# Kernel optimization log

Hardware: AMD Instinct MI355X
Metric: run time of the kernel (lower is better)

The kernel has to match this reference:

```python
import jax, jax.numpy as jnp
from jax import lax
import numpy as np

B, C, T = 16, 512, 4096
COEFF_INIT = 0.04


def setup_inputs() -> dict:
    key = jax.random.key(0)
    k1, k2 = jax.random.split(key)
    x = jax.random.normal(k1, (B, C, T), dtype=jnp.float32)
    # learned per-channel smoothing coefficients, initialized like the module
    weights = jnp.ones((C,), dtype=jnp.float32) * COEFF_INIT
    return {"x": x, "weights": weights}


def reference(x, weights):
    # clamp weights to [0, 1] (mirrors the in-place no-grad clamp; values stay
    # unchanged here since coeff_init is inside the range)
    s = jnp.clip(weights, 0.0, 1.0)  # [C]
    xt = jnp.moveaxis(x, 2, 0)       # [T, B, C]
    init = xt[0]                      # y_0 = x_0

    def step(acc, sample):
        acc = s * sample + (1.0 - s) * acc
        return acc, acc

    _, ys = lax.scan(step, init, xt[1:])          # [T-1, B, C]
    out = jnp.concatenate([init[None], ys], axis=0)  # [T, B, C]
    return jnp.moveaxis(out, 0, 2)                   # [B, C, T]
```

## Files before the change

kernel.cpp:

```cpp
#include <hip/hip_runtime.h>


constexpr int T_LEN = 4096;
constexpr int C_LEN = 512;
constexpr int BLOCK = 256;
constexpr int PER_THREAD = T_LEN / BLOCK;

__global__ __launch_bounds__(BLOCK) void ema_scan_kernel(
    const float* __restrict__ x,
    const float* __restrict__ w,
    float* __restrict__ y)
{
    const int row  = blockIdx.x;
    const int c    = row & (C_LEN - 1);
    const int tid  = threadIdx.x;
    const int lane = tid & 63;
    const int wave = tid >> 6;

    float s = w[c];
    s = fminf(fmaxf(s, 0.0f), 1.0f);
    const float a = 1.0f - s;

    const float* xr = x + (size_t)row * T_LEN + tid * PER_THREAD;
    float*       yr = y + (size_t)row * T_LEN + tid * PER_THREAD;

    float4 v0 = ((const float4*)xr)[0];
    float4 v1 = ((const float4*)xr)[1];
    float4 v2 = ((const float4*)xr)[2];
    float4 v3 = ((const float4*)xr)[3];

    float l[PER_THREAD];
    l[0]=v0.x; l[1]=v0.y; l[2]=v0.z;  l[3]=v0.w;
    l[4]=v1.x; l[5]=v1.y; l[6]=v1.z;  l[7]=v1.w;
    l[8]=v2.x; l[9]=v2.y; l[10]=v2.z; l[11]=v2.w;
    l[12]=v3.x;l[13]=v3.y;l[14]=v3.z; l[15]=v3.w;

    float acc = (tid == 0) ? l[0] : s * l[0];
    l[0] = acc;
    #pragma unroll
    for (int j = 1; j < PER_THREAD; ++j) {
        float t = s * l[j];
        acc = fmaf(a, acc, t);
        l[j] = acc;
    }

    float a2 = a * a;
    float a4 = a2 * a2;
    float a8 = a4 * a4;
    const float a16 = a8 * a8;

    float S = acc;
    float wgt = a16;
    #pragma unroll
    for (int d = 1; d < 64; d <<= 1) {
        float up = __shfl_up(S, d, 64);
        if (lane >= d) S = fmaf(wgt, up, S);
        wgt *= wgt;
    }

    __shared__ float tot[4];
    if (lane == 63) tot[wave] = S;
    __syncthreads();

    float a64 = a16;
    #pragma unroll
    for (int k = 0; k < 6; ++k) a64 *= a64;

    float Cw = 0.0f;
    {
        float f = 1.0f;
        for (int u = wave - 1; u >= 0; --u) {
            Cw = fmaf(f, tot[u], Cw);
            f *= a64;
        }
    }

    float Sx = __shfl_up(S, 1, 64);
    float P_local = (lane == 0) ? 0.0f : Sx;
    float powl = 1.0f, tq = a16;
    #pragma unroll
    for (int bit = 0; bit < 6; ++bit) {
        if ((lane >> bit) & 1) powl *= tq;
        tq *= tq;
    }
    const float P = fmaf(powl, Cw, P_local);

    float aj = a;
    #pragma unroll
    for (int j = 0; j < PER_THREAD; ++j) {
        l[j] = fmaf(aj, P, l[j]);
        aj *= a;
    }

    float4 o0 = make_float4(l[0],  l[1],  l[2],  l[3]);
    float4 o1 = make_float4(l[4],  l[5],  l[6],  l[7]);
    float4 o2 = make_float4(l[8],  l[9],  l[10], l[11]);
    float4 o3 = make_float4(l[12], l[13], l[14], l[15]);
    ((float4*)yr)[0] = o0;
    ((float4*)yr)[1] = o1;
    ((float4*)yr)[2] = o2;
    ((float4*)yr)[3] = o3;
}

extern "C" void kernel_launch(void* const* d_in, const int* in_sizes, int n_in,
                              void* d_out, int out_size, void* d_ws, size_t ws_size,
                              hipStream_t stream) {
    const float* x = (const float*)d_in[0];
    const float* w = (const float*)d_in[1];
    float* y = (float*)d_out;

    const int rows = out_size / T_LEN;
    ema_scan_kernel<<<rows, BLOCK, 0, stream>>>(x, w, y);
}
```

Before: 232.8 us.

## Use 1024-thread blocks with one float4 per thread for fully coalesced scan

Each row is now handled by 1024 threads, each loading and storing one contiguous float4, in place of 256 threads each handling 16 elements. This makes every global access coalesced across the wave, where the old per-thread strided float4 loads were not. The cost is a longer serial cross-wave prefix over 16 wave totals and block-wide sync at higher thread count. The wave-level shuffle scan weights are recomputed for 4-element chunks.

```diff
diff --git a/kernel.cpp b/kernel.cpp
--- a/kernel.cpp
+++ b/kernel.cpp
@@ -3,8 +3,8 @@
 
 constexpr int T_LEN = 4096;
 constexpr int C_LEN = 512;
-constexpr int BLOCK = 256;
-constexpr int PER_THREAD = T_LEN / BLOCK;
+constexpr int BLOCK = 1024;
+constexpr int NWAVES = BLOCK / 64;
 
 __global__ __launch_bounds__(BLOCK) void ema_scan_kernel(
     const float* __restrict__ x,
@@ -21,85 +21,59 @@
     s = fminf(fmaxf(s, 0.0f), 1.0f);
     const float a = 1.0f - s;
 
-    const float* xr = x + (size_t)row * T_LEN + tid * PER_THREAD;
-    float*       yr = y + (size_t)row * T_LEN + tid * PER_THREAD;
+    const float4* xr = (const float4*)(x + (size_t)row * T_LEN) + tid;
+    float4*       yr = (float4*)(y + (size_t)row * T_LEN) + tid;
 
-    float4 v0 = ((const float4*)xr)[0];
-    float4 v1 = ((const float4*)xr)[1];
-    float4 v2 = ((const float4*)xr)[2];
-    float4 v3 = ((const float4*)xr)[3];
+    float4 v = *xr;
 
-    float l[PER_THREAD];
-    l[0]=v0.x; l[1]=v0.y; l[2]=v0.z;  l[3]=v0.w;
-    l[4]=v1.x; l[5]=v1.y; l[6]=v1.z;  l[7]=v1.w;
-    l[8]=v2.x; l[9]=v2.y; l[10]=v2.z; l[11]=v2.w;
-    l[12]=v3.x;l[13]=v3.y;l[14]=v3.z; l[15]=v3.w;
+    float l0 = (tid == 0) ? v.x : s * v.x;
+    float l1 = fmaf(a, l0, s * v.y);
+    float l2 = fmaf(a, l1, s * v.z);
+    float l3 = fmaf(a, l2, s * v.w);
 
-    float acc = (tid == 0) ? l[0] : s * l[0];
-    l[0] = acc;
-    #pragma unroll
-    for (int j = 1; j < PER_THREAD; ++j) {
-        float t = s * l[j];
-        acc = fmaf(a, acc, t);
-        l[j] = acc;
-    }
+    const float a2 = a * a;
+    const float a3 = a2 * a;
+    const float a4 = a2 * a2;
 
-    float a2 = a * a;
-    float a4 = a2 * a2;
-    float a8 = a4 * a4;
-    const float a16 = a8 * a8;
-
-    float S = acc;
-    float wgt = a16;
+    float S = l3;
+    float wgt = a4;
     #pragma unroll
     for (int d = 1; d < 64; d <<= 1) {
         float up = __shfl_up(S, d, 64);
         if (lane >= d) S = fmaf(wgt, up, S);
         wgt *= wgt;
     }
+    const float a256 = wgt;
 
-    __shared__ float tot[4];
+    __shared__ float tot[NWAVES];
     if (lane == 63) tot[wave] = S;
     __syncthreads();
-
-    float a64 = a16;
-    #pragma unroll
-    for (int k = 0; k < 6; ++k) a64 *= a64;
 
     float Cw = 0.0f;
     {
         float f = 1.0f;
         for (int u = wave - 1; u >= 0; --u) {
             Cw = fmaf(f, tot[u], Cw);
-            f *= a64;
+            f *= a256;
         }
     }
 
     float Sx = __shfl_up(S, 1, 64);
-    float P_local = (lane == 0) ? 0.0f : Sx;
-    float powl = 1.0f, tq = a16;
+    float Pl = (lane == 0) ? 0.0f : Sx;
+    float powl = 1.0f, tq = a4;
     #pragma unroll
-    for (int bit = 0; bit < 6; ++bit) {
-        if ((lane >> bit) & 1) powl *= tq;
+    for (int b = 0; b < 6; ++b) {
+        if ((lane >> b) & 1) powl *= tq;
         tq *= tq;
     }
-    const float P = fmaf(powl, Cw, P_local);
+    const float P = fmaf(powl, Cw, Pl);
 
-    float aj = a;
-    #pragma unroll
-    for (int j = 0; j < PER_THREAD; ++j) {
-        l[j] = fmaf(aj, P, l[j]);
-        aj *= a;
-    }
-
-    float4 o0 = make_float4(l[0],  l[1],  l[2],  l[3]);
-    float4 o1 = make_float4(l[4],  l[5],  l[6],  l[7]);
-    float4 o2 = make_float4(l[8],  l[9],  l[10], l[11]);
-    float4 o3 = make_float4(l[12], l[13], l[14], l[15]);
-    ((float4*)yr)[0] = o0;
-    ((float4*)yr)[1] = o1;
-    ((float4*)yr)[2] = o2;
-    ((float4*)yr)[3] = o3;
+    float4 o;
+    o.x = fmaf(a,  P, l0);
+    o.y = fmaf(a2, P, l1);
+    o.z = fmaf(a3, P, l2);
+    o.w = fmaf(a4, P, l3);
+    *yr = o;
 }
 
 extern "C" void kernel_launch(void* const* d_in, const int* in_sizes, int n_in,
@@ -110,5 +84,5 @@
     float* y = (float*)d_out;
 
     const int rows = out_size / T_LEN;
-    ema_scan_kernel<<<rows, BLOCK, 0, stream>>>(x, w, y);
+    ema_scan_kernel<<<rows, BLOCK, 0, stream>>>(x, y != nullptr ? w : w, y);
 }
```

Measured after the change: 224.1 us. 3.7% less time.
